# Optimization experiments

Measured on AMD Instinct MI355X. Metric: run time of the kernel, lower is better.

The kernel has to match this reference:

```python
import jax, jax.numpy as jnp
import numpy as np

N = 27  # input_size == hidden_size == 27 (hardcoded in source)


def setup_inputs() -> dict:
    key = jax.random.key(0)
    ks = jax.random.split(key, 10)
    B, T = 2048, 1024
    s_ih = 1.0 / np.sqrt(N)
    inp = {
        "x": jax.random.normal(ks[0], (B, T, N), dtype=jnp.float32),
        "h0": jax.random.normal(ks[1], (1, B, N), dtype=jnp.float32),
        "c0": jax.random.normal(ks[2], (1, B, N), dtype=jnp.float32),
        # LSTM params, PyTorch layout: [4H, in], gate order (i, f, g, o)
        "W_ih": jax.random.uniform(ks[3], (4 * N, N), jnp.float32, -s_ih, s_ih),
        "W_hh": jax.random.uniform(ks[4], (4 * N, N), jnp.float32, -s_ih, s_ih),
        "b_ih": jax.random.uniform(ks[5], (4 * N,), jnp.float32, -s_ih, s_ih),
        "b_hh": jax.random.uniform(ks[6], (4 * N,), jnp.float32, -s_ih, s_ih),
        # i2o Linear 27 -> 27
        "W_out": jax.random.uniform(ks[7], (N, N), jnp.float32, -s_ih, s_ih),
        "b_out": jax.random.uniform(ks[8], (N,), jnp.float32, -s_ih, s_ih),
    }
    return inp


def lstm_forward(x, h0, c0, W_ih, W_hh, b_ih, b_hh):
    # x: [B, T, N]; h0/c0: [B, H]
    H = h0.shape[-1]
    # Precompute input contribution for all timesteps: [T, B, 4H]
    xg = jnp.einsum("btn,gn->tbg", x, W_ih) + (b_ih + b_hh)

    def step(carry, xg_t):
        h, c = carry
        z = xg_t + h @ W_hh.T  # [B, 4H]
        i = jax.nn.sigmoid(z[:, 0 * H:1 * H])
        f = jax.nn.sigmoid(z[:, 1 * H:2 * H])
        g = jnp.tanh(z[:, 2 * H:3 * H])
        o = jax.nn.sigmoid(z[:, 3 * H:4 * H])
        c_new = f * c + i * g
        h_new = o * jnp.tanh(c_new)
        return (h_new, c_new), h_new

    (hn, cn), hs = jax.lax.scan(step, (h0, c0), xg)
    return jnp.transpose(hs, (1, 0, 2)), hn, cn  # [B, T, H], [B, H], [B, H]


def reference(x, h0, c0, W_ih, W_hh, b_ih, b_hh, W_out, b_out):
    hs, hn, cn = lstm_forward(x, h0[0], c0[0], W_ih, W_hh, b_ih, b_hh)
    out = hs @ W_out.T + b_out  # i2o projection, [B, T, N]
    return out, (hn[None], cn[None])
```

## Files before the change

### kernel.cpp

```cpp
#include <hip/hip_runtime.h>
#include <cstdint>

constexpr int Bb = 2048;
constexpr int Tt = 1024;
constexpr int Nn = 27;

__device__ __forceinline__ float rcpf(float a) { return __builtin_amdgcn_rcpf(a); }

__global__ __launch_bounds__(64, 1) void lstm_fused_kernel(
    const float* __restrict__ x,
    const float* __restrict__ h0,
    const float* __restrict__ c0,
    const float* __restrict__ W_ih,
    const float* __restrict__ W_hh,
    const float* __restrict__ b_ih,
    const float* __restrict__ b_hh,
    const float* __restrict__ W_out,
    const float* __restrict__ b_out,
    float* __restrict__ out,
    float* __restrict__ hn,
    float* __restrict__ cn)
{
    const int tid = threadIdx.x;
    const int bl  = tid >> 5;
    const int j   = tid & 31;
    const bool act = (j < Nn);
    const int jj  = act ? j : (Nn - 1);
    const int bg  = (int)blockIdx.x * 2 + bl;

    __shared__ __align__(16) float xbuf[2][2][32];
    __shared__ __align__(16) float hbuf[2][2][32];

    float wih[4][28], whh[4][28], wout[28];
#pragma unroll
    for (int g = 0; g < 4; ++g) {
#pragma unroll
        for (int k = 0; k < 28; ++k) {
            wih[g][k] = (k < Nn) ? W_ih[(g * Nn + jj) * Nn + k] : 0.0f;
            whh[g][k] = (k < Nn) ? W_hh[(g * Nn + jj) * Nn + k] : 0.0f;
        }
    }
#pragma unroll
    for (int k = 0; k < 28; ++k)
        wout[k] = (k < Nn) ? W_out[jj * Nn + k] : 0.0f;

    const float bz0 = b_ih[0 * Nn + jj] + b_hh[0 * Nn + jj];
    const float bz1 = b_ih[1 * Nn + jj] + b_hh[1 * Nn + jj];
    const float bz2 = b_ih[2 * Nn + jj] + b_hh[2 * Nn + jj];
    const float bz3 = b_ih[3 * Nn + jj] + b_hh[3 * Nn + jj];
    const float bo  = b_out[jj];

    float c  = c0[(size_t)bg * Nn + jj];
    float hv = h0[(size_t)bg * Nn + jj];

    const float* xrow = x   + (size_t)bg * Tt * Nn + jj;
    float*       orow = out + (size_t)bg * Tt * Nn + j;

    hbuf[0][bl][j] = act ? hv : 0.0f;
    xbuf[0][bl][j] = act ? xrow[0] : 0.0f;
    __builtin_amdgcn_wave_barrier();
    float xn1 = act ? xrow[Nn] : 0.0f;

#pragma unroll 2
    for (int t = 0; t < Tt; ++t) {
        const int cur = t & 1;
        const int nxt = cur ^ 1;

        xbuf[nxt][bl][j] = act ? xn1 : 0.0f;
        __builtin_amdgcn_wave_barrier();

        int t2 = t + 2; t2 = (t2 < Tt) ? t2 : (Tt - 1);
        const float xn2 = act ? xrow[(size_t)t2 * Nn] : 0.0f;

        const float4* hq = (const float4*)(&hbuf[cur][bl][0]);
        const float4* xq = (const float4*)(&xbuf[cur][bl][0]);
        const float4 h0q = hq[0], h1q = hq[1], h2q = hq[2], h3q = hq[3],
                     h4q = hq[4], h5q = hq[5], h6q = hq[6];
        const float4 x0q = xq[0], x1q = xq[1], x2q = xq[2], x3q = xq[3],
                     x4q = xq[4], x5q = xq[5], x6q = xq[6];

        float z0 = bz0, z1 = bz1, z2 = bz2, z3 = bz3;
        float oacc = bo;

        {
            const float4 xv[7] = {x0q, x1q, x2q, x3q, x4q, x5q, x6q};
#pragma unroll
            for (int q = 0; q < 7; ++q) {
                const float4 v = xv[q];
                z0 = fmaf(wih[0][4*q+0], v.x, z0); z0 = fmaf(wih[0][4*q+1], v.y, z0);
                z0 = fmaf(wih[0][4*q+2], v.z, z0); z0 = fmaf(wih[0][4*q+3], v.w, z0);
                z1 = fmaf(wih[1][4*q+0], v.x, z1); z1 = fmaf(wih[1][4*q+1], v.y, z1);
                z1 = fmaf(wih[1][4*q+2], v.z, z1); z1 = fmaf(wih[1][4*q+3], v.w, z1);
                z2 = fmaf(wih[2][4*q+0], v.x, z2); z2 = fmaf(wih[2][4*q+1], v.y, z2);
                z2 = fmaf(wih[2][4*q+2], v.z, z2); z2 = fmaf(wih[2][4*q+3], v.w, z2);
                z3 = fmaf(wih[3][4*q+0], v.x, z3); z3 = fmaf(wih[3][4*q+1], v.y, z3);
                z3 = fmaf(wih[3][4*q+2], v.z, z3); z3 = fmaf(wih[3][4*q+3], v.w, z3);
            }
        }

        {
            const float4 hv4[7] = {h0q, h1q, h2q, h3q, h4q, h5q, h6q};
#pragma unroll
            for (int q = 0; q < 7; ++q) {
                const float4 v = hv4[q];
                z0 = fmaf(whh[0][4*q+0], v.x, z0); z0 = fmaf(whh[0][4*q+1], v.y, z0);
                z0 = fmaf(whh[0][4*q+2], v.z, z0); z0 = fmaf(whh[0][4*q+3], v.w, z0);
                z1 = fmaf(whh[1][4*q+0], v.x, z1); z1 = fmaf(whh[1][4*q+1], v.y, z1);
                z1 = fmaf(whh[1][4*q+2], v.z, z1); z1 = fmaf(whh[1][4*q+3], v.w, z1);
                z2 = fmaf(whh[2][4*q+0], v.x, z2); z2 = fmaf(whh[2][4*q+1], v.y, z2);
                z2 = fmaf(whh[2][4*q+2], v.z, z2); z2 = fmaf(whh[2][4*q+3], v.w, z2);
                z3 = fmaf(whh[3][4*q+0], v.x, z3); z3 = fmaf(whh[3][4*q+1], v.y, z3);
                z3 = fmaf(whh[3][4*q+2], v.z, z3); z3 = fmaf(whh[3][4*q+3], v.w, z3);
                oacc = fmaf(wout[4*q+0], v.x, oacc); oacc = fmaf(wout[4*q+1], v.y, oacc);
                oacc = fmaf(wout[4*q+2], v.z, oacc); oacc = fmaf(wout[4*q+3], v.w, oacc);
            }
        }

        if (t > 0 && act) orow[(size_t)(t - 1) * Nn] = oacc;

        const float e0 = __expf(-z0);
        const float e1 = __expf(-z1);
        const float e2 = __expf(2.0f * z2);
        const float e3 = __expf(-z3);
        const float ig = rcpf(1.0f + e0);
        const float fg = rcpf(1.0f + e1);
        const float gg = 1.0f - 2.0f * rcpf(1.0f + e2);
        const float og = rcpf(1.0f + e3);
        c = fmaf(fg, c, ig * gg);
        const float tc = 1.0f - 2.0f * rcpf(1.0f + __expf(2.0f * c));
        hv = og * tc;

        hbuf[nxt][bl][j] = act ? hv : 0.0f;
        __builtin_amdgcn_wave_barrier();
        xn1 = xn2;
    }

    {
        float oacc = bo;
        const float4* hq = (const float4*)(&hbuf[Tt & 1][bl][0]);
#pragma unroll
        for (int q = 0; q < 7; ++q) {
            const float4 v = hq[q];
            oacc = fmaf(wout[4*q+0], v.x, oacc); oacc = fmaf(wout[4*q+1], v.y, oacc);
            oacc = fmaf(wout[4*q+2], v.z, oacc); oacc = fmaf(wout[4*q+3], v.w, oacc);
        }
        if (act) {
            orow[(size_t)(Tt - 1) * Nn] = oacc;
            hn[(size_t)bg * Nn + j] = hv;
            cn[(size_t)bg * Nn + j] = c;
        }
    }
}

extern "C" void kernel_launch(void* const* d_in, const int* in_sizes, int n_in,
                              void* d_out, int out_size, void* d_ws, size_t ws_size,
                              hipStream_t stream) {
    const float* x     = (const float*)d_in[0];
    const float* h0    = (const float*)d_in[1];
    const float* c0    = (const float*)d_in[2];
    const float* W_ih  = (const float*)d_in[3];
    const float* W_hh  = (const float*)d_in[4];
    const float* b_ih  = (const float*)d_in[5];
    const float* b_hh  = (const float*)d_in[6];
    const float* W_out = (const float*)d_in[7];
    const float* b_out = (const float*)d_in[8];

    float* out = (float*)d_out;
    float* hn  = out + (size_t)Bb * Tt * Nn;
    float* cn  = hn + (size_t)Bb * Nn;

    lstm_fused_kernel<<<dim3(Bb / 2), dim3(64), 0, stream>>>(
        x, h0, c0, W_ih, W_hh, b_ih, b_hh, W_out, b_out, out, hn, cn);
}
```

Before: 1.058 ms.

## Split the K reduction across wave halves, one batch per wave, and precompute x-gates ahead

Each wavefront now handles one batch row instead of two, and its two 32-lane halves each reduce half of the 27-element input and hidden dot products, combined with a cross-half shuffle. The input-projection contribution for the next step is computed off the critical path after the state update. The x prefetch distance grows to three steps. Launch bounds now allow two blocks per CU and the grid doubles. The aim is to halve per-lane serial FMA work and register pressure on the recurrent critical path. The cost is shuffle latency every step and twice as many waves.

```diff
diff --git a/kernel.cpp b/kernel.cpp
--- a/kernel.cpp
+++ b/kernel.cpp
@@ -4,10 +4,11 @@
 constexpr int Bb = 2048;
 constexpr int Tt = 1024;
 constexpr int Nn = 27;
+constexpr int KH = 16;
 
 __device__ __forceinline__ float rcpf(float a) { return __builtin_amdgcn_rcpf(a); }
 
-__global__ __launch_bounds__(64, 1) void lstm_fused_kernel(
+__global__ __launch_bounds__(64, 2) void lstm_fused_kernel(
     const float* __restrict__ x,
     const float* __restrict__ h0,
     const float* __restrict__ c0,
@@ -21,87 +22,97 @@
     float* __restrict__ hn,
     float* __restrict__ cn)
 {
-    const int tid = threadIdx.x;
-    const int bl  = tid >> 5;
-    const int j   = tid & 31;
+    const int lane = threadIdx.x;
+    const int j    = lane & 31;
+    const int half = lane >> 5;
+    const int k0   = half * KH;
     const bool act = (j < Nn);
-    const int jj  = act ? j : (Nn - 1);
-    const int bg  = (int)blockIdx.x * 2 + bl;
-
-    __shared__ __align__(16) float xbuf[2][2][32];
-    __shared__ __align__(16) float hbuf[2][2][32];
-
-    float wih[4][28], whh[4][28], wout[28];
+    const bool pub = (lane < Nn);
+    const int jj   = act ? j : (Nn - 1);
+    const int bg   = blockIdx.x;
+
+    __shared__ __align__(16) float xbuf[2][32];
+    __shared__ __align__(16) float hbuf[2][32];
+
+    float wih[4][KH], whh[4][KH], wout[KH];
 #pragma unroll
     for (int g = 0; g < 4; ++g) {
 #pragma unroll
-        for (int k = 0; k < 28; ++k) {
-            wih[g][k] = (k < Nn) ? W_ih[(g * Nn + jj) * Nn + k] : 0.0f;
-            whh[g][k] = (k < Nn) ? W_hh[(g * Nn + jj) * Nn + k] : 0.0f;
-        }
-    }
-#pragma unroll
-    for (int k = 0; k < 28; ++k)
-        wout[k] = (k < Nn) ? W_out[jj * Nn + k] : 0.0f;
-
-    const float bz0 = b_ih[0 * Nn + jj] + b_hh[0 * Nn + jj];
-    const float bz1 = b_ih[1 * Nn + jj] + b_hh[1 * Nn + jj];
-    const float bz2 = b_ih[2 * Nn + jj] + b_hh[2 * Nn + jj];
-    const float bz3 = b_ih[3 * Nn + jj] + b_hh[3 * Nn + jj];
-    const float bo  = b_out[jj];
+        for (int kk = 0; kk < KH; ++kk) {
+            const int k = k0 + kk;
+            wih[g][kk] = (k < Nn) ? W_ih[(g * Nn + jj) * Nn + k] : 0.0f;
+            whh[g][kk] = (k < Nn) ? W_hh[(g * Nn + jj) * Nn + k] : 0.0f;
+        }
+    }
+#pragma unroll
+    for (int kk = 0; kk < KH; ++kk) {
+        const int k = k0 + kk;
+        wout[kk] = (k < Nn) ? W_out[jj * Nn + k] : 0.0f;
+    }
+
+    const float bz0 = (half == 0) ? b_ih[0 * Nn + jj] + b_hh[0 * Nn + jj] : 0.0f;
+    const float bz1 = (half == 0) ? b_ih[1 * Nn + jj] + b_hh[1 * Nn + jj] : 0.0f;
+    const float bz2 = (half == 0) ? b_ih[2 * Nn + jj] + b_hh[2 * Nn + jj] : 0.0f;
+    const float bz3 = (half == 0) ? b_ih[3 * Nn + jj] + b_hh[3 * Nn + jj] : 0.0f;
+    const float bo  = (half == 0) ? b_out[jj] : 0.0f;
 
     float c  = c0[(size_t)bg * Nn + jj];
     float hv = h0[(size_t)bg * Nn + jj];
 
-    const float* xrow = x   + (size_t)bg * Tt * Nn + jj;
-    float*       orow = out + (size_t)bg * Tt * Nn + j;
-
-    hbuf[0][bl][j] = act ? hv : 0.0f;
-    xbuf[0][bl][j] = act ? xrow[0] : 0.0f;
+    const float* xrow = x   + (size_t)bg * Tt * Nn;
+    float*       orow = out + (size_t)bg * Tt * Nn;
+
+    if (lane < 32) {
+        xbuf[0][j] = act ? xrow[j] : 0.0f;
+        hbuf[0][j] = act ? hv : 0.0f;
+        xbuf[1][j] = 0.0f;
+        hbuf[1][j] = 0.0f;
+    }
     __builtin_amdgcn_wave_barrier();
-    float xn1 = act ? xrow[Nn] : 0.0f;
+
+    float xn1 = pub ? xrow[1 * Nn + j] : 0.0f;
+    float xn2 = pub ? xrow[2 * Nn + j] : 0.0f;
+
+    float zx0, zx1, zx2, zx3;
+    {
+        const float4* xq = (const float4*)(&xbuf[0][k0]);
+        const float4 v0 = xq[0], v1 = xq[1], v2 = xq[2], v3 = xq[3];
+        const float4 xv[4] = {v0, v1, v2, v3};
+        zx0 = bz0; zx1 = bz1; zx2 = bz2; zx3 = bz3;
+#pragma unroll
+        for (int q = 0; q < 4; ++q) {
+            const float4 v = xv[q];
+            zx0 = fmaf(wih[0][4*q+0], v.x, zx0); zx0 = fmaf(wih[0][4*q+1], v.y, zx0);
+            zx0 = fmaf(wih[0][4*q+2], v.z, zx0); zx0 = fmaf(wih[0][4*q+3], v.w, zx0);
+            zx1 = fmaf(wih[1][4*q+0], v.x, zx1); zx1 = fmaf(wih[1][4*q+1], v.y, zx1);
+            zx1 = fmaf(wih[1][4*q+2], v.z, zx1); zx1 = fmaf(wih[1][4*q+3], v.w, zx1);
+            zx2 = fmaf(wih[2][4*q+0], v.x, zx2); zx2 = fmaf(wih[2][4*q+1], v.y, zx2);
+            zx2 = fmaf(wih[2][4*q+2], v.z, zx2); zx2 = fmaf(wih[2][4*q+3], v.w, zx2);
+            zx3 = fmaf(wih[3][4*q+0], v.x, zx3); zx3 = fmaf(wih[3][4*q+1], v.y, zx3);
+            zx3 = fmaf(wih[3][4*q+2], v.z, zx3); zx3 = fmaf(wih[3][4*q+3], v.w, zx3);
+        }
+    }
 
 #pragma unroll 2
     for (int t = 0; t < Tt; ++t) {
         const int cur = t & 1;
         const int nxt = cur ^ 1;
 
-        xbuf[nxt][bl][j] = act ? xn1 : 0.0f;
+        if (pub) xbuf[nxt][j] = xn1;
         __builtin_amdgcn_wave_barrier();
 
-        int t2 = t + 2; t2 = (t2 < Tt) ? t2 : (Tt - 1);
-        const float xn2 = act ? xrow[(size_t)t2 * Nn] : 0.0f;
-
-        const float4* hq = (const float4*)(&hbuf[cur][bl][0]);
-        const float4* xq = (const float4*)(&xbuf[cur][bl][0]);
-        const float4 h0q = hq[0], h1q = hq[1], h2q = hq[2], h3q = hq[3],
-                     h4q = hq[4], h5q = hq[5], h6q = hq[6];
-        const float4 x0q = xq[0], x1q = xq[1], x2q = xq[2], x3q = xq[3],
-                     x4q = xq[4], x5q = xq[5], x6q = xq[6];
-
-        float z0 = bz0, z1 = bz1, z2 = bz2, z3 = bz3;
+        int t3 = t + 3; t3 = (t3 < Tt) ? t3 : (Tt - 1);
+        const float xnew = pub ? xrow[(size_t)t3 * Nn + j] : 0.0f;
+
+        const float4* hq = (const float4*)(&hbuf[cur][k0]);
+        const float4 h0q = hq[0], h1q = hq[1], h2q = hq[2], h3q = hq[3];
+
+        float z0 = zx0, z1 = zx1, z2 = zx2, z3 = zx3;
         float oacc = bo;
-
         {
-            const float4 xv[7] = {x0q, x1q, x2q, x3q, x4q, x5q, x6q};
-#pragma unroll
-            for (int q = 0; q < 7; ++q) {
-                const float4 v = xv[q];
-                z0 = fmaf(wih[0][4*q+0], v.x, z0); z0 = fmaf(wih[0][4*q+1], v.y, z0);
-                z0 = fmaf(wih[0][4*q+2], v.z, z0); z0 = fmaf(wih[0][4*q+3], v.w, z0);
-                z1 = fmaf(wih[1][4*q+0], v.x, z1); z1 = fmaf(wih[1][4*q+1], v.y, z1);
-                z1 = fmaf(wih[1][4*q+2], v.z, z1); z1 = fmaf(wih[1][4*q+3], v.w, z1);
-                z2 = fmaf(wih[2][4*q+0], v.x, z2); z2 = fmaf(wih[2][4*q+1], v.y, z2);
-                z2 = fmaf(wih[2][4*q+2], v.z, z2); z2 = fmaf(wih[2][4*q+3], v.w, z2);
-                z3 = fmaf(wih[3][4*q+0], v.x, z3); z3 = fmaf(wih[3][4*q+1], v.y, z3);
-                z3 = fmaf(wih[3][4*q+2], v.z, z3); z3 = fmaf(wih[3][4*q+3], v.w, z3);
-            }
-        }
-
-        {
-            const float4 hv4[7] = {h0q, h1q, h2q, h3q, h4q, h5q, h6q};
-#pragma unroll
-            for (int q = 0; q < 7; ++q) {
+            const float4 hv4[4] = {h0q, h1q, h2q, h3q};
+#pragma unroll
+            for (int q = 0; q < 4; ++q) {
                 const float4 v = hv4[q];
                 z0 = fmaf(whh[0][4*q+0], v.x, z0); z0 = fmaf(whh[0][4*q+1], v.y, z0);
                 z0 = fmaf(whh[0][4*q+2], v.z, z0); z0 = fmaf(whh[0][4*q+3], v.w, z0);
@@ -116,7 +127,13 @@
             }
         }
 
-        if (t > 0 && act) orow[(size_t)(t - 1) * Nn] = oacc;
+        z0 += __shfl_xor(z0, 32);
+        z1 += __shfl_xor(z1, 32);
+        z2 += __shfl_xor(z2, 32);
+        z3 += __shfl_xor(z3, 32);
+        oacc += __shfl_xor(oacc, 32);
+
+        if (t > 0 && pub) orow[(size_t)(t - 1) * Nn + j] = oacc;
 
         const float e0 = __expf(-z0);
         const float e1 = __expf(-z1);
@@ -130,22 +147,45 @@
         const float tc = 1.0f - 2.0f * rcpf(1.0f + __expf(2.0f * c));
         hv = og * tc;
 
-        hbuf[nxt][bl][j] = act ? hv : 0.0f;
+        {
+            const float4* xq = (const float4*)(&xbuf[nxt][k0]);
+            const float4 v0 = xq[0], v1 = xq[1], v2 = xq[2], v3 = xq[3];
+            const float4 xv[4] = {v0, v1, v2, v3};
+            zx0 = bz0; zx1 = bz1; zx2 = bz2; zx3 = bz3;
+#pragma unroll
+            for (int q = 0; q < 4; ++q) {
+                const float4 v = xv[q];
+                zx0 = fmaf(wih[0][4*q+0], v.x, zx0); zx0 = fmaf(wih[0][4*q+1], v.y, zx0);
+                zx0 = fmaf(wih[0][4*q+2], v.z, zx0); zx0 = fmaf(wih[0][4*q+3], v.w, zx0);
+                zx1 = fmaf(wih[1][4*q+0], v.x, zx1); zx1 = fmaf(wih[1][4*q+1], v.y, zx1);
+                zx1 = fmaf(wih[1][4*q+2], v.z, zx1); zx1 = fmaf(wih[1][4*q+3], v.w, zx1);
+                zx2 = fmaf(wih[2][4*q+0], v.x, zx2); zx2 = fmaf(wih[2][4*q+1], v.y, zx2);
+                zx2 = fmaf(wih[2][4*q+2], v.z, zx2); zx2 = fmaf(wih[2][4*q+3], v.w, zx2);
+                zx3 = fmaf(wih[3][4*q+0], v.x, zx3); zx3 = fmaf(wih[3][4*q+1], v.y, zx3);
+                zx3 = fmaf(wih[3][4*q+2], v.z, zx3); zx3 = fmaf(wih[3][4*q+3], v.w, zx3);
+            }
+        }
+
+        if (pub) hbuf[nxt][j] = hv;
         __builtin_amdgcn_wave_barrier();
         xn1 = xn2;
+        xn2 = xnew;
     }
 
     {
+        const float4* hq = (const float4*)(&hbuf[0][k0]);
+        const float4 h0q = hq[0], h1q = hq[1], h2q = hq[2], h3q = hq[3];
+        const float4 hv4[4] = {h0q, h1q, h2q, h3q};
         float oacc = bo;
-        const float4* hq = (const float4*)(&hbuf[Tt & 1][bl][0]);
-#pragma unroll
-        for (int q = 0; q < 7; ++q) {
-            const float4 v = hq[q];
+#pragma unroll
+        for (int q = 0; q < 4; ++q) {
+            const float4 v = hv4[q];
             oacc = fmaf(wout[4*q+0], v.x, oacc); oacc = fmaf(wout[4*q+1], v.y, oacc);
             oacc = fmaf(wout[4*q+2], v.z, oacc); oacc = fmaf(wout[4*q+3], v.w, oacc);
         }
-        if (act) {
-            orow[(size_t)(Tt - 1) * Nn] = oacc;
+        oacc += __shfl_xor(oacc, 32);
+        if (pub) {
+            orow[(size_t)(Tt - 1) * Nn + j] = oacc;
             hn[(size_t)bg * Nn + j] = hv;
             cn[(size_t)bg * Nn + j] = c;
         }
@@ -169,6 +209,6 @@
     float* hn  = out + (size_t)Bb * Tt * Nn;
     float* cn  = hn + (size_t)Bb * Nn;
 
-    lstm_fused_kernel<<<dim3(Bb / 2), dim3(64), 0, stream>>>(
+    lstm_fused_kernel<<<dim3(Bb), dim3(64), 0, stream>>>(
         x, h0, c0, W_ih, W_hh, b_ih, b_hh, W_out, b_out, out, hn, cn);
 }
```

Measured after the change: 951.7 us. 1.11x faster.
